# Kernel optimization log

Hardware: AMD Instinct MI355X
Metric: run time of the kernel (lower is better)

Reference implementation:

```python
import jax, jax.numpy as jnp
import numpy as np

D_MODEL, N_HEADS, D_HEAD = 1024, 16, 64
IGNORE = -1e5

def setup_inputs() -> dict:
    key = jax.random.key(0)
    ks = jax.random.split(key, 5)
    std = 0.02
    return {
        "resid_pre": jax.random.normal(ks[0], (4, 2048, D_MODEL), dtype=jnp.float32),
        "W_Q": jax.random.normal(ks[1], (N_HEADS, D_MODEL, D_HEAD), dtype=jnp.float32) * std,
        "W_K": jax.random.normal(ks[2], (N_HEADS, D_MODEL, D_HEAD), dtype=jnp.float32) * std,
        "W_V": jax.random.normal(ks[3], (N_HEADS, D_MODEL, D_HEAD), dtype=jnp.float32) * std,
        "W_O": jax.random.normal(ks[4], (N_HEADS, D_HEAD, D_MODEL), dtype=jnp.float32) * std,
        "b_Q": jnp.zeros((N_HEADS, D_HEAD), dtype=jnp.float32),
        "b_K": jnp.zeros((N_HEADS, D_HEAD), dtype=jnp.float32),
        "b_V": jnp.zeros((N_HEADS, D_HEAD), dtype=jnp.float32),
        "b_O": jnp.zeros((D_MODEL,), dtype=jnp.float32),
    }

def reference(resid_pre, W_Q, W_K, W_V, W_O, b_Q, b_K, b_V, b_O):
    # q/k/v: [batch, posn, n_heads, d_head]
    q = jnp.einsum("hmd,bsm->bshd", W_Q, resid_pre) + b_Q
    k = jnp.einsum("hmd,bsm->bshd", W_K, resid_pre) + b_K
    v = jnp.einsum("hmd,bsm->bshd", W_V, resid_pre) + b_V
    # scores: [batch, n_heads, posn_q, posn_k]
    scores = jnp.einsum("bqhd,bkhd->bhqk", q, k) / jnp.sqrt(jnp.float32(D_HEAD))
    S = resid_pre.shape[1]
    causal = jnp.tril(jnp.ones((S, S), dtype=bool))  # keep where True
    scores = jnp.where(causal, scores, jnp.float32(IGNORE))
    probs = jax.nn.softmax(scores, axis=-1)
    z = jnp.einsum("bhqk,bkhd->bqhd", probs, v)  # [batch, posn_q, n_heads, d_head]
    # project each head to d_model and sum over heads, then add b_O
    attn_out = jnp.einsum("hdm,bqhd->bqm", W_O, z) + b_O
    return attn_out
```

## Files before the change

### kernel.cpp

```cpp
#include <hip/hip_runtime.h>

typedef __bf16 bf16;
typedef __attribute__((ext_vector_type(8))) __bf16 bf16x8;
typedef __attribute__((ext_vector_type(4))) float f32x4;

__device__ __forceinline__ void gload_lds16(const void* g, void* l) {
  __builtin_amdgcn_global_load_lds(
      (const __attribute__((address_space(1))) unsigned int*)(g),
      (__attribute__((address_space(3))) unsigned int*)(l),
      16, 0, 0);
}

__device__ __forceinline__ float exp2_hw(float x) {
  float r; asm("v_exp_f32 %0, %1" : "=v"(r) : "v"(x)); return r;
}
__device__ __forceinline__ unsigned cvtpk_bf16(float a, float b) {
  unsigned r; asm("v_cvt_pk_bf16_f32 %0, %1, %2" : "=v"(r) : "v"(a), "v"(b)); return r;
}


__global__ __launch_bounds__(256) void pack_x(const float* __restrict__ x, bf16* __restrict__ o) {
  int i = (blockIdx.x * 256 + threadIdx.x) * 8;
  float4 a = *(const float4*)(x + i);
  float4 b = *(const float4*)(x + i + 4);
  bf16x8 v;
  v[0] = (bf16)a.x; v[1] = (bf16)a.y; v[2] = (bf16)a.z; v[3] = (bf16)a.w;
  v[4] = (bf16)b.x; v[5] = (bf16)b.y; v[6] = (bf16)b.z; v[7] = (bf16)b.w;
  *(bf16x8*)(o + i) = v;
}

__global__ __launch_bounds__(256) void pack_w(const float* __restrict__ WQ, const float* __restrict__ WK,
                                              const float* __restrict__ WV, bf16* __restrict__ Wt) {
  int bid = blockIdx.x;
  int p = bid >> 8, h = (bid >> 4) & 15, k0 = (bid & 15) * 64;
  const float* src = (p == 0 ? WQ : p == 1 ? WK : WV) + h * 65536;
  __shared__ float tile[64][65];
  int t = threadIdx.x, c = t & 63, r4 = t >> 6;
#pragma unroll
  for (int rr = 0; rr < 16; ++rr) {
    int k = r4 + rr * 4;
    tile[k][c] = src[(k0 + k) * 64 + c];
  }
  __syncthreads();
#pragma unroll
  for (int rr = 0; rr < 16; ++rr) {
    int d = r4 + rr * 4;
    Wt[(p * 1024 + h * 64 + d) * 1024 + k0 + c] = (bf16)tile[c][d];
  }
}

__global__ __launch_bounds__(256) void pack_wo(const float* __restrict__ WO, bf16* __restrict__ Wt) {
  int bid = blockIdx.x;
  int r0 = (bid >> 4) * 64, c0 = (bid & 15) * 64;
  __shared__ float tile[64][65];
  int t = threadIdx.x, c = t & 63, r4 = t >> 6;
#pragma unroll
  for (int rr = 0; rr < 16; ++rr) {
    int r = r4 + rr * 4;
    tile[r][c] = WO[(r0 + r) * 1024 + c0 + c];
  }
  __syncthreads();
#pragma unroll
  for (int rr = 0; rr < 16; ++rr) {
    int m = r4 + rr * 4;
    Wt[(c0 + m) * 1024 + r0 + c] = (bf16)tile[c][m];
  }
}

__global__ __launch_bounds__(256) void pack_bias(const float* __restrict__ bQ, const float* __restrict__ bK,
                                                 const float* __restrict__ bV, float* __restrict__ o) {
  int i = blockIdx.x * 256 + threadIdx.x;
  if (i < 3072) {
    int p = i >> 10, j = i & 1023;
    o[i] = (p == 0 ? bQ : p == 1 ? bK : bV)[j];
  }
}

template <int OUTF32>
__global__ __launch_bounds__(256, 2) void gemm_bt(const bf16* __restrict__ A, const bf16* __restrict__ Bt,
                                                  const float* __restrict__ bias, void* __restrict__ Cv,
                                                  int M, int N, int K) {
  __shared__ bf16 As[128 * 64];
  __shared__ bf16 Bs[128 * 64];
  int tid = threadIdx.x;
  int wv = tid >> 6, ln = tid & 63, lr = ln & 15, lh = ln >> 4;
  int wr = wv >> 1, wc = wv & 1;
  int row0 = blockIdx.y * 128, col0 = blockIdx.x * 128;
  int ss = (ln & 7) ^ (ln >> 3);
  const char* ga = (const char*)(A + (long)(row0 + wv * 32 + (ln >> 3)) * K) + ss * 16;
  const char* gb = (const char*)(Bt + (long)(col0 + wv * 32 + (ln >> 3)) * K) + ss * 16;
  long rowskip = (long)8 * K * 2;
  f32x4 acc[4][4] = {};
  for (int k0 = 0; k0 < K; k0 += 64) {
#pragma unroll
    for (int i = 0; i < 4; ++i) {
      gload_lds16(ga + (long)k0 * 2 + i * rowskip, (char*)As + (wv * 32 + i * 8) * 128);
      gload_lds16(gb + (long)k0 * 2 + i * rowskip, (char*)Bs + (wv * 32 + i * 8) * 128);
    }
    __syncthreads();
    bf16x8 af[4][2], bfr[4][2];
#pragma unroll
    for (int mi = 0; mi < 4; ++mi)
#pragma unroll
      for (int ks = 0; ks < 2; ++ks) {
        int row = wr * 64 + mi * 16 + lr;
        int o = row * 128 + (((ks * 4 + lh) ^ (row & 7)) << 4);
        af[mi][ks] = *(const bf16x8*)((const char*)As + o);
      }
#pragma unroll
    for (int ni = 0; ni < 4; ++ni)
#pragma unroll
      for (int ks = 0; ks < 2; ++ks) {
        int row = wc * 64 + ni * 16 + lr;
        int o = row * 128 + (((ks * 4 + lh) ^ (row & 7)) << 4);
        bfr[ni][ks] = *(const bf16x8*)((const char*)Bs + o);
      }
    __builtin_amdgcn_s_setprio(1);
#pragma unroll
    for (int ks = 0; ks < 2; ++ks)
#pragma unroll
      for (int mi = 0; mi < 4; ++mi)
#pragma unroll
        for (int ni = 0; ni < 4; ++ni)
          acc[mi][ni] = __builtin_amdgcn_mfma_f32_16x16x32_bf16(af[mi][ks], bfr[ni][ks], acc[mi][ni], 0, 0, 0);
    __builtin_amdgcn_s_setprio(0);
    __syncthreads();
  }
#pragma unroll
  for (int mi = 0; mi < 4; ++mi) {
    int row = row0 + wr * 64 + mi * 16 + lh * 4;
#pragma unroll
    for (int ni = 0; ni < 4; ++ni) {
      int col = col0 + wc * 64 + ni * 16 + lr;
      float bvv = bias[col];
#pragma unroll
      for (int r = 0; r < 4; ++r) {
        float v = acc[mi][ni][r] + bvv;
        if (OUTF32) ((float*)Cv)[(long)(row + r) * N + col] = v;
        else        ((bf16*)Cv)[(long)(row + r) * N + col] = (bf16)v;
      }
    }
  }
}

__global__ __launch_bounds__(256, 2) void flash(const bf16* __restrict__ Qkv, bf16* __restrict__ Z) {
  __shared__ bf16 Vt[2][64 * 64];
  __shared__ unsigned char Pl[4][4096];
  const float SCALE = 0.1803368867f;
  const float MASKV = -144269.5041f;
  int bid = blockIdx.x;
  int qt = 15 - (bid >> 6);
  int bh = (bid & 7) * 8 + ((bid >> 3) & 7);
  int b = bh >> 4, h = bh & 15;
  int tid = threadIdx.x;
  int wv = tid >> 6, ln = tid & 63, lr = ln & 15, lh = ln >> 4;
  int q0 = qt * 128;
  const bf16* Qg = Qkv + (long)b * 2048 * 3072 + h * 64;
  const bf16* Kg = Qg + 1024;
  const bf16* Vg = Qg + 2048;
  int nt = 2 * (qt + 1);
  int vs0 = (tid >> 3) * 2, vd0 = (tid & 7) * 8;

  bf16x8 v0, v1;
  auto loadV = [&](int kvrow0) {
    v0 = *(const bf16x8*)(Vg + (long)(kvrow0 + vs0) * 3072 + vd0);
    v1 = *(const bf16x8*)(Vg + (long)(kvrow0 + vs0 + 1) * 3072 + vd0);
  };
  auto writeV = [&](bf16* vd) {
#pragma unroll
    for (int j = 0; j < 8; ++j) {
      int d = vd0 + j;
      int o = (d * 128 + vs0 * 2) ^ ((((d & 7) ^ (d >> 3)) & 7) << 4);
      unsigned int pk = (unsigned int)__builtin_bit_cast(unsigned short, (bf16)v0[j])
                      | ((unsigned int)__builtin_bit_cast(unsigned short, (bf16)v1[j]) << 16);
      *(unsigned int*)((char*)vd + o) = pk;
    }
  };

  bf16x8 bq[2][2];
#pragma unroll
  for (int mi = 0; mi < 2; ++mi)
#pragma unroll
    for (int ks = 0; ks < 2; ++ks)
      bq[mi][ks] = *(const bf16x8*)(Qg + (long)(q0 + wv * 32 + mi * 16 + lr) * 3072 + ks * 32 + lh * 8);
  loadV(0);
  writeV(Vt[0]);
  __syncthreads();

  f32x4 oa[4][2] = {};
  float m_st[2], l_st[2];
  m_st[0] = m_st[1] = -1e30f;
  l_st[0] = l_st[1] = 0.f;
  char* pw = (char*)Pl[wv];

  int cur = 0;
  for (int t = 0; t < nt; ++t) {
    int kv0 = t * 64;
    bool more = (t + 1 < nt);
    bf16x8 kf[4][2];
#pragma unroll
    for (int n = 0; n < 4; ++n)
#pragma unroll
      for (int ks = 0; ks < 2; ++ks)
        kf[n][ks] = *(const bf16x8*)(Kg + (long)(kv0 + n * 16 + lr) * 3072 + ks * 32 + lh * 8);
    if (more) loadV(kv0 + 64);
    f32x4 sc[2][4];
    __builtin_amdgcn_s_setprio(1);
#pragma unroll
    for (int mi = 0; mi < 2; ++mi)
#pragma unroll
      for (int n = 0; n < 4; ++n) {
        f32x4 zacc = {0.f, 0.f, 0.f, 0.f};
        zacc = __builtin_amdgcn_mfma_f32_16x16x32_bf16(kf[n][0], bq[mi][0], zacc, 0, 0, 0);
        zacc = __builtin_amdgcn_mfma_f32_16x16x32_bf16(kf[n][1], bq[mi][1], zacc, 0, 0, 0);
        sc[mi][n] = zacc;
      }
    __builtin_amdgcn_s_setprio(0);
    bool domask = (kv0 + 63 > q0);
#pragma unroll
    for (int mi = 0; mi < 2; ++mi) {
      int qrow = q0 + wv * 32 + mi * 16 + lr;
#pragma unroll
      for (int n = 0; n < 4; ++n) {
        int kvb = kv0 + n * 16 + lh * 4;
#pragma unroll
        for (int r = 0; r < 4; ++r) {
          float v = sc[mi][n][r] * SCALE;
          if (domask && (kvb + r > qrow)) v = MASKV;
          sc[mi][n][r] = v;
        }
      }
    }
#pragma unroll
    for (int mi = 0; mi < 2; ++mi) {
      float mx = sc[mi][0][0];
#pragma unroll
      for (int n = 0; n < 4; ++n)
#pragma unroll
        for (int r = 0; r < 4; ++r) mx = fmaxf(mx, sc[mi][n][r]);
      mx = fmaxf(mx, __shfl_xor(mx, 16));
      mx = fmaxf(mx, __shfl_xor(mx, 32));
      float mn = fmaxf(m_st[mi], mx);
      float resc = exp2_hw(m_st[mi] - mn);
      m_st[mi] = mn;
      float s = 0.f;
#pragma unroll
      for (int n = 0; n < 4; ++n)
#pragma unroll
        for (int r = 0; r < 4; ++r) {
          float p = exp2_hw(sc[mi][n][r] - mn);
          sc[mi][n][r] = p;
          s += p;
        }
      s += __shfl_xor(s, 16);
      s += __shfl_xor(s, 32);
      l_st[mi] = l_st[mi] * resc + s;
#pragma unroll
      for (int n2 = 0; n2 < 4; ++n2)
#pragma unroll
        for (int r = 0; r < 4; ++r) oa[n2][mi][r] *= resc;
    }
#pragma unroll
    for (int mi = 0; mi < 2; ++mi) {
      int row = mi * 16 + lr;
#pragma unroll
      for (int n = 0; n < 4; ++n) {
        int addr = row * 128 + ((n * 32 + lh * 8) ^ ((row & 7) << 4));
        uint2 val = { cvtpk_bf16(sc[mi][n][0], sc[mi][n][1]),
                      cvtpk_bf16(sc[mi][n][2], sc[mi][n][3]) };
        *(uint2*)(pw + addr) = val;
      }
    }
    if (more) writeV(Vt[cur ^ 1]);
    bf16x8 pa[2][2];
#pragma unroll
    for (int mi = 0; mi < 2; ++mi)
#pragma unroll
      for (int ks = 0; ks < 2; ++ks) {
        int row = mi * 16 + lr;
        int o = row * 128 + (((ks * 4 + lh) ^ (row & 7)) << 4);
        pa[mi][ks] = *(const bf16x8*)(pw + o);
      }
    __builtin_amdgcn_s_setprio(1);
#pragma unroll
    for (int n2 = 0; n2 < 4; ++n2) {
      int row = n2 * 16 + lr;
      int o0 = row * 128 + ((((0 + lh) ^ (row & 7) ^ ((row >> 3) & 7)) & 7) << 4);
      int o1 = row * 128 + ((((4 + lh) ^ (row & 7) ^ ((row >> 3) & 7)) & 7) << 4);
      bf16x8 vf0 = *(const bf16x8*)((const char*)Vt[cur] + o0);
      bf16x8 vf1 = *(const bf16x8*)((const char*)Vt[cur] + o1);
#pragma unroll
      for (int mi = 0; mi < 2; ++mi) {
        oa[n2][mi] = __builtin_amdgcn_mfma_f32_16x16x32_bf16(vf0, pa[mi][0], oa[n2][mi], 0, 0, 0);
        oa[n2][mi] = __builtin_amdgcn_mfma_f32_16x16x32_bf16(vf1, pa[mi][1], oa[n2][mi], 0, 0, 0);
      }
    }
    __builtin_amdgcn_s_setprio(0);
    __syncthreads();
    cur ^= 1;
  }
#pragma unroll
  for (int mi = 0; mi < 2; ++mi) {
    float inv = 1.0f / l_st[mi];
    int q = q0 + wv * 32 + mi * 16 + lr;
    bf16* zb = Z + ((long)b * 2048 + q) * 1024 + h * 64 + lh * 4;
#pragma unroll
    for (int n2 = 0; n2 < 4; ++n2) {
      uint2 o2 = { cvtpk_bf16(oa[n2][mi][0] * inv, oa[n2][mi][1] * inv),
                   cvtpk_bf16(oa[n2][mi][2] * inv, oa[n2][mi][3] * inv) };
      *(uint2*)(zb + n2 * 16) = o2;
    }
  }
}

extern "C" void kernel_launch(void* const* d_in, const int* in_sizes, int n_in,
                              void* d_out, int out_size, void* d_ws, size_t ws_size,
                              hipStream_t stream) {
  const float* resid = (const float*)d_in[0];
  const float* WQ = (const float*)d_in[1];
  const float* WK = (const float*)d_in[2];
  const float* WV = (const float*)d_in[3];
  const float* WO = (const float*)d_in[4];
  const float* bQ = (const float*)d_in[5];
  const float* bK = (const float*)d_in[6];
  const float* bV = (const float*)d_in[7];
  const float* bO = (const float*)d_in[8];
  char* ws = (char*)d_ws;
  bf16*  Xb      = (bf16*)ws;
  bf16*  Z       = (bf16*)ws;
  bf16*  Wqkv    = (bf16*)(ws + 16777216);
  bf16*  Wot     = (bf16*)(ws + 16777216);
  float* biasqkv = (float*)(ws + 23068672);
  bf16*  QKVo    = (bf16*)(ws + 23085056);

  pack_x<<<4096, 256, 0, stream>>>(resid, Xb);
  pack_w<<<768, 256, 0, stream>>>(WQ, WK, WV, Wqkv);
  pack_bias<<<12, 256, 0, stream>>>(bQ, bK, bV, biasqkv);
  gemm_bt<0><<<dim3(24, 64), 256, 0, stream>>>(Xb, Wqkv, biasqkv, QKVo, 8192, 3072, 1024);
  pack_wo<<<256, 256, 0, stream>>>(WO, Wot);
  flash<<<1024, 256, 0, stream>>>(QKVo, Z);
  gemm_bt<1><<<dim3(8, 64), 256, 0, stream>>>(Z, Wot, bO, d_out, 8192, 1024, 1024);
}
```

Measured before the change: 283.1 us.

## Restructure flash attention into paired 64-row query tiles with lazy rescaling

The flash kernel now handles 64-row query tiles with one 16-row slice per wave, and each block processes a pair of tiles (pair and 31-pair) so causal work is balanced across blocks. Occupancy is raised to 4 blocks per SU through launch bounds and a halved P buffer. Masking is applied only on the diagonal tile, and the online-softmax rescale is skipped unless the max grows by more than 8 in the log2 domain. In exchange, each K/V tile is reused by half as many query rows, so global K/V traffic roughly doubles. The lazy rescale also lets exponentials reach up to 2^8 before renormalising.

Measured after the change: 323.4 us. 1.14x slower.

```diff
diff --git a/kernel.cpp b/kernel.cpp
--- a/kernel.cpp
+++ b/kernel.cpp
@@ -143,23 +143,22 @@
   }
 }
 
-__global__ __launch_bounds__(256, 2) void flash(const bf16* __restrict__ Qkv, bf16* __restrict__ Z) {
+__global__ __launch_bounds__(256, 4) void flash(const bf16* __restrict__ Qkv, bf16* __restrict__ Z) {
   __shared__ bf16 Vt[2][64 * 64];
-  __shared__ unsigned char Pl[4][4096];
+  __shared__ unsigned char Pl[4][2048];
   const float SCALE = 0.1803368867f;
   const float MASKV = -144269.5041f;
   int bid = blockIdx.x;
-  int qt = 15 - (bid >> 6);
+  int pair = bid >> 6;
   int bh = (bid & 7) * 8 + ((bid >> 3) & 7);
   int b = bh >> 4, h = bh & 15;
   int tid = threadIdx.x;
   int wv = tid >> 6, ln = tid & 63, lr = ln & 15, lh = ln >> 4;
-  int q0 = qt * 128;
   const bf16* Qg = Qkv + (long)b * 2048 * 3072 + h * 64;
   const bf16* Kg = Qg + 1024;
   const bf16* Vg = Qg + 2048;
-  int nt = 2 * (qt + 1);
   int vs0 = (tid >> 3) * 2, vd0 = (tid & 7) * 8;
+  char* pw = (char*)Pl[wv];
 
   bf16x8 v0, v1;
   auto loadV = [&](int kvrow0) {
@@ -177,137 +176,121 @@
     }
   };
 
-  bf16x8 bq[2][2];
-#pragma unroll
-  for (int mi = 0; mi < 2; ++mi)
+#pragma unroll 1
+  for (int half = 0; half < 2; ++half) {
+    int qt = half ? 31 - pair : pair;
+    int q0 = qt * 64;
+    int nt = qt + 1;
+    loadV(0);
+    bf16x8 bq[2];
 #pragma unroll
     for (int ks = 0; ks < 2; ++ks)
-      bq[mi][ks] = *(const bf16x8*)(Qg + (long)(q0 + wv * 32 + mi * 16 + lr) * 3072 + ks * 32 + lh * 8);
-  loadV(0);
-  writeV(Vt[0]);
-  __syncthreads();
-
-  f32x4 oa[4][2] = {};
-  float m_st[2], l_st[2];
-  m_st[0] = m_st[1] = -1e30f;
-  l_st[0] = l_st[1] = 0.f;
-  char* pw = (char*)Pl[wv];
-
-  int cur = 0;
-  for (int t = 0; t < nt; ++t) {
-    int kv0 = t * 64;
-    bool more = (t + 1 < nt);
-    bf16x8 kf[4][2];
-#pragma unroll
-    for (int n = 0; n < 4; ++n)
-#pragma unroll
-      for (int ks = 0; ks < 2; ++ks)
-        kf[n][ks] = *(const bf16x8*)(Kg + (long)(kv0 + n * 16 + lr) * 3072 + ks * 32 + lh * 8);
-    if (more) loadV(kv0 + 64);
-    f32x4 sc[2][4];
-    __builtin_amdgcn_s_setprio(1);
-#pragma unroll
-    for (int mi = 0; mi < 2; ++mi)
+      bq[ks] = *(const bf16x8*)(Qg + (long)(q0 + wv * 16 + lr) * 3072 + ks * 32 + lh * 8);
+    writeV(Vt[0]);
+    __syncthreads();
+
+    f32x4 oa[4] = {};
+    float m_st = -1e30f, l_st = 0.f;
+    int cur = 0;
+    for (int t = 0; t < nt; ++t) {
+      int kv0 = t * 64;
+      bool more = (t + 1 < nt);
+      bf16x8 kf[4][2];
+#pragma unroll
+      for (int n = 0; n < 4; ++n)
+#pragma unroll
+        for (int ks = 0; ks < 2; ++ks)
+          kf[n][ks] = *(const bf16x8*)(Kg + (long)(kv0 + n * 16 + lr) * 3072 + ks * 32 + lh * 8);
+      if (more) loadV(kv0 + 64);
+      f32x4 sc[4];
+      __builtin_amdgcn_s_setprio(1);
 #pragma unroll
       for (int n = 0; n < 4; ++n) {
         f32x4 zacc = {0.f, 0.f, 0.f, 0.f};
-        zacc = __builtin_amdgcn_mfma_f32_16x16x32_bf16(kf[n][0], bq[mi][0], zacc, 0, 0, 0);
-        zacc = __builtin_amdgcn_mfma_f32_16x16x32_bf16(kf[n][1], bq[mi][1], zacc, 0, 0, 0);
-        sc[mi][n] = zacc;
-      }
-    __builtin_amdgcn_s_setprio(0);
-    bool domask = (kv0 + 63 > q0);
-#pragma unroll
-    for (int mi = 0; mi < 2; ++mi) {
-      int qrow = q0 + wv * 32 + mi * 16 + lr;
-#pragma unroll
-      for (int n = 0; n < 4; ++n) {
-        int kvb = kv0 + n * 16 + lh * 4;
-#pragma unroll
-        for (int r = 0; r < 4; ++r) {
-          float v = sc[mi][n][r] * SCALE;
-          if (domask && (kvb + r > qrow)) v = MASKV;
-          sc[mi][n][r] = v;
+        zacc = __builtin_amdgcn_mfma_f32_16x16x32_bf16(kf[n][0], bq[0], zacc, 0, 0, 0);
+        zacc = __builtin_amdgcn_mfma_f32_16x16x32_bf16(kf[n][1], bq[1], zacc, 0, 0, 0);
+        sc[n] = zacc;
+      }
+      __builtin_amdgcn_s_setprio(0);
+#pragma unroll
+      for (int n = 0; n < 4; ++n)
+#pragma unroll
+        for (int r = 0; r < 4; ++r) sc[n][r] *= SCALE;
+      if (t == nt - 1) {
+        int qrow = q0 + wv * 16 + lr;
+#pragma unroll
+        for (int n = 0; n < 4; ++n) {
+          int kvb = kv0 + n * 16 + lh * 4;
+#pragma unroll
+          for (int r = 0; r < 4; ++r)
+            if (kvb + r > qrow) sc[n][r] = MASKV;
         }
       }
-    }
-#pragma unroll
-    for (int mi = 0; mi < 2; ++mi) {
-      float mx = sc[mi][0][0];
+      float mx = sc[0][0];
 #pragma unroll
       for (int n = 0; n < 4; ++n)
 #pragma unroll
-        for (int r = 0; r < 4; ++r) mx = fmaxf(mx, sc[mi][n][r]);
+        for (int r = 0; r < 4; ++r) mx = fmaxf(mx, sc[n][r]);
       mx = fmaxf(mx, __shfl_xor(mx, 16));
       mx = fmaxf(mx, __shfl_xor(mx, 32));
-      float mn = fmaxf(m_st[mi], mx);
-      float resc = exp2_hw(m_st[mi] - mn);
-      m_st[mi] = mn;
+      if (!__all(mx <= m_st + 8.0f)) {
+        float mn = fmaxf(m_st, mx);
+        float resc = exp2_hw(m_st - mn);
+        m_st = mn;
+        l_st *= resc;
+#pragma unroll
+        for (int n2 = 0; n2 < 4; ++n2)
+#pragma unroll
+          for (int r = 0; r < 4; ++r) oa[n2][r] *= resc;
+      }
       float s = 0.f;
 #pragma unroll
       for (int n = 0; n < 4; ++n)
 #pragma unroll
         for (int r = 0; r < 4; ++r) {
-          float p = exp2_hw(sc[mi][n][r] - mn);
-          sc[mi][n][r] = p;
+          float p = exp2_hw(sc[n][r] - m_st);
+          sc[n][r] = p;
           s += p;
         }
       s += __shfl_xor(s, 16);
       s += __shfl_xor(s, 32);
-      l_st[mi] = l_st[mi] * resc + s;
-#pragma unroll
-      for (int n2 = 0; n2 < 4; ++n2)
-#pragma unroll
-        for (int r = 0; r < 4; ++r) oa[n2][mi][r] *= resc;
-    }
-#pragma unroll
-    for (int mi = 0; mi < 2; ++mi) {
-      int row = mi * 16 + lr;
+      l_st += s;
 #pragma unroll
       for (int n = 0; n < 4; ++n) {
-        int addr = row * 128 + ((n * 32 + lh * 8) ^ ((row & 7) << 4));
-        uint2 val = { cvtpk_bf16(sc[mi][n][0], sc[mi][n][1]),
-                      cvtpk_bf16(sc[mi][n][2], sc[mi][n][3]) };
+        int addr = lr * 128 + ((n * 32 + lh * 8) ^ ((lr & 7) << 4));
+        uint2 val = { cvtpk_bf16(sc[n][0], sc[n][1]),
+                      cvtpk_bf16(sc[n][2], sc[n][3]) };
         *(uint2*)(pw + addr) = val;
       }
-    }
-    if (more) writeV(Vt[cur ^ 1]);
-    bf16x8 pa[2][2];
-#pragma unroll
-    for (int mi = 0; mi < 2; ++mi)
+      if (more) writeV(Vt[cur ^ 1]);
+      bf16x8 pa[2];
 #pragma unroll
       for (int ks = 0; ks < 2; ++ks) {
-        int row = mi * 16 + lr;
-        int o = row * 128 + (((ks * 4 + lh) ^ (row & 7)) << 4);
-        pa[mi][ks] = *(const bf16x8*)(pw + o);
-      }
-    __builtin_amdgcn_s_setprio(1);
+        int o = lr * 128 + (((ks * 4 + lh) ^ (lr & 7)) << 4);
+        pa[ks] = *(const bf16x8*)(pw + o);
+      }
+      __builtin_amdgcn_s_setprio(1);
+#pragma unroll
+      for (int n2 = 0; n2 < 4; ++n2) {
+        int row = n2 * 16 + lr;
+        int o0 = row * 128 + ((((0 + lh) ^ (row & 7) ^ ((row >> 3) & 7)) & 7) << 4);
+        int o1 = row * 128 + ((((4 + lh) ^ (row & 7) ^ ((row >> 3) & 7)) & 7) << 4);
+        bf16x8 vf0 = *(const bf16x8*)((const char*)Vt[cur] + o0);
+        bf16x8 vf1 = *(const bf16x8*)((const char*)Vt[cur] + o1);
+        oa[n2] = __builtin_amdgcn_mfma_f32_16x16x32_bf16(vf0, pa[0], oa[n2], 0, 0, 0);
+        oa[n2] = __builtin_amdgcn_mfma_f32_16x16x32_bf16(vf1, pa[1], oa[n2], 0, 0, 0);
+      }
+      __builtin_amdgcn_s_setprio(0);
+      __syncthreads();
+      cur ^= 1;
+    }
+    float inv = 1.0f / l_st;
+    int q = q0 + wv * 16 + lr;
+    bf16* zb = Z + ((long)b * 2048 + q) * 1024 + h * 64 + lh * 4;
 #pragma unroll
     for (int n2 = 0; n2 < 4; ++n2) {
-      int row = n2 * 16 + lr;
-      int o0 = row * 128 + ((((0 + lh) ^ (row & 7) ^ ((row >> 3) & 7)) & 7) << 4);
-      int o1 = row * 128 + ((((4 + lh) ^ (row & 7) ^ ((row >> 3) & 7)) & 7) << 4);
-      bf16x8 vf0 = *(const bf16x8*)((const char*)Vt[cur] + o0);
-      bf16x8 vf1 = *(const bf16x8*)((const char*)Vt[cur] + o1);
-#pragma unroll
-      for (int mi = 0; mi < 2; ++mi) {
-        oa[n2][mi] = __builtin_amdgcn_mfma_f32_16x16x32_bf16(vf0, pa[mi][0], oa[n2][mi], 0, 0, 0);
-        oa[n2][mi] = __builtin_amdgcn_mfma_f32_16x16x32_bf16(vf1, pa[mi][1], oa[n2][mi], 0, 0, 0);
-      }
-    }
-    __builtin_amdgcn_s_setprio(0);
-    __syncthreads();
-    cur ^= 1;
-  }
-#pragma unroll
-  for (int mi = 0; mi < 2; ++mi) {
-    float inv = 1.0f / l_st[mi];
-    int q = q0 + wv * 32 + mi * 16 + lr;
-    bf16* zb = Z + ((long)b * 2048 + q) * 1024 + h * 64 + lh * 4;
-#pragma unroll
-    for (int n2 = 0; n2 < 4; ++n2) {
-      uint2 o2 = { cvtpk_bf16(oa[n2][mi][0] * inv, oa[n2][mi][1] * inv),
-                   cvtpk_bf16(oa[n2][mi][2] * inv, oa[n2][mi][3] * inv) };
+      uint2 o2 = { cvtpk_bf16(oa[n2][0] * inv, oa[n2][1] * inv),
+                   cvtpk_bf16(oa[n2][2] * inv, oa[n2][3] * inv) };
       *(uint2*)(zb + n2 * 16) = o2;
     }
   }
```
